# Optimization experiments

Hardware: AMD Instinct MI355X
Metric: run time of the kernel (lower is better)

## Reference

```python
import jax, jax.numpy as jnp
import numpy as np

N, D, V, T = 1024, 64, 32000, 2048
U_DECAY = 0.97
LN_EPS = 1e-6


def _layernorm_row(z):
    # matches torch: (z - mean) / (std_unbiased + eps), std uses ddof=1
    m = z.mean(axis=-1, keepdims=True)
    s = jnp.std(z, axis=-1, ddof=1, keepdims=True)
    return (z - m) / (s + LN_EPS)


def setup_inputs() -> dict:
    key = jax.random.key(0)
    k1, k2, k3, k4, k5 = jax.random.split(key, 5)
    E = jax.random.normal(k1, (D, N), dtype=jnp.float32) / np.float32(np.sqrt(N))
    Dx = jax.random.normal(k2, (N, D), dtype=jnp.float32) / np.float32(np.sqrt(D))
    Dy = jax.random.normal(k3, (N, D), dtype=jnp.float32) / np.float32(np.sqrt(D))
    token_emb = jax.random.normal(k4, (V, D), dtype=jnp.float32) / np.float32(np.sqrt(D))
    tokens = jax.random.randint(k5, (T,), 0, V, dtype=jnp.int32)
    x0 = jnp.zeros((N,), dtype=jnp.float32)
    rho0 = jnp.zeros((D, N), dtype=jnp.float32)
    return {"E": E, "Dx": Dx, "Dy": Dy, "token_emb": token_emb,
            "x0": x0, "rho0": rho0, "tokens": tokens}


def reference(E, Dx, Dy, token_emb, x0, rho0, tokens):
    def step(carry, tok):
        x, rho = carry                        # x: [N], rho: [D, N]
        v_prev = token_emb[tok]               # [D]
        x_t = x + jax.nn.relu(Dx @ v_prev)    # [N], use_relu_lowrank=True
        a_star = rho @ x_t                    # [D]
        y_core = Dy @ _layernorm_row(a_star)  # ln_before_Dy=True -> [N]
        y_t = jax.nn.relu(y_core) * jax.nn.relu(x_t)  # [N]
        v_star = _layernorm_row(E @ y_t)      # [D]
        rho_new = U_DECAY * (rho + jnp.outer(v_prev, x_t))  # [D, N]
        return (x_t, rho_new), (y_t, v_star)

    (_, _), (ys, vs) = jax.lax.scan(step, (x0, rho0), tokens)
    return ys, vs  # [T, N], [T, D]
```

## Files before the change

### kernel.cpp

```cpp
#include <hip/hip_runtime.h>
#include <math.h>

#define NN 1024
#define DD 64
#define TT 2048
#define UDEC 0.97f
#define EPS 1e-6f

#define CC 64
#define NCH 32
#define NSL 16
#define SLW 64
#define C2 8
#define NC2 256

#define NTHR 256

__device__ __forceinline__ int swz4(int r, int c4) { return r * 16 + (c4 ^ (r & 15)); }

#define DOT4(p, q2) ((p).x*(q2).x + (p).y*(q2).y + (p).z*(q2).z + (p).w*(q2).w)
#define F4ADD(a, b) make_float4((a).x+(b).x, (a).y+(b).y, (a).z+(b).z, (a).w+(b).w)

__global__ __launch_bounds__(NTHR) void k_prep(
    const float* __restrict__ E, float* __restrict__ Et4,
    const float* __restrict__ Dx, float* __restrict__ Dxq,
    const float* __restrict__ Dy, float* __restrict__ Dyq)
{
    const int b = blockIdx.x, tid = threadIdx.x;
    if (b < 64) {
        const int fi = b * NTHR + tid;
        const int n4 = fi >> 6, d = fi & 63;
        reinterpret_cast<float4*>(Et4)[fi] =
            reinterpret_cast<const float4*>(E)[d * (NN / 4) + n4];
    } else if (b < 128) {
        const int fi = (b - 64) * NTHR + tid;
        const int d4 = fi >> 10, n = fi & 1023;
        reinterpret_cast<float4*>(Dxq)[fi] =
            reinterpret_cast<const float4*>(Dx)[n * (DD / 4) + d4];
    } else {
        const int fi = (b - 128) * NTHR + tid;
        const int d4 = fi >> 10, n = fi & 1023;
        reinterpret_cast<float4*>(Dyq)[fi] =
            reinterpret_cast<const float4*>(Dy)[n * (DD / 4) + d4];
    }
}

__global__ __launch_bounds__(NTHR) void k_xscan(
    const float* __restrict__ Dxq, const float* __restrict__ temb,
    const int* __restrict__ toks, float* __restrict__ Xp, float* __restrict__ S)
{
    __shared__ float Vs[C2][DD];
    const int b = blockIdx.x, tid = threadIdx.x;
    const int cs = b >> 2, qx = b & 3;
    const int n = qx * 256 + tid;
    for (int i = tid; i < C2 * DD / 4; i += NTHR) {
        int s = i >> 4, d4 = i & 15;
        reinterpret_cast<float4*>(&Vs[s][0])[d4] =
            reinterpret_cast<const float4*>(temb + toks[cs * C2 + s] * DD)[d4];
    }
    __syncthreads();
    float dxr[DD];
    const float4* dxq4 = reinterpret_cast<const float4*>(Dxq);
#pragma unroll
    for (int j = 0; j < 16; ++j) {
        float4 v = dxq4[j * NN + n];
        dxr[4*j] = v.x; dxr[4*j+1] = v.y; dxr[4*j+2] = v.z; dxr[4*j+3] = v.w;
    }
    float run = 0.f;
    for (int s = 0; s < C2; ++s) {
        const float4* vr = reinterpret_cast<const float4*>(&Vs[s][0]);
        float a0 = 0.f, a1 = 0.f, a2 = 0.f, a3 = 0.f;
#pragma unroll
        for (int j = 0; j < 16; ++j) {
            float4 v = vr[j];
            a0 += v.x * dxr[4*j];     a1 += v.y * dxr[4*j+1];
            a2 += v.z * dxr[4*j+2];   a3 += v.w * dxr[4*j+3];
        }
        run += fmaxf((a0 + a1) + (a2 + a3), 0.f);
        Xp[(cs * C2 + s) * NN + n] = run;
    }
    S[cs * NN + n] = run;
}

__global__ __launch_bounds__(NTHR) void k_base(
    const float* __restrict__ S, const float* __restrict__ x0, float* __restrict__ Bb)
{
    __shared__ float ssl[8][33];
    const int b = blockIdx.x, tid = threadIdx.x;
    const int n_l = tid & 31, seg = tid >> 5;
    const int n = b * 32 + n_l;
    float m[32];
#pragma unroll
    for (int j = 0; j < 32; ++j) m[j] = S[(seg * 32 + j) * NN + n];
    float tot = 0.f;
#pragma unroll
    for (int j = 0; j < 32; ++j) tot += m[j];
    ssl[seg][n_l] = tot;
    __syncthreads();
    float acc = x0[n];
    for (int r = 0; r < seg; ++r) acc += ssl[r][n_l];
#pragma unroll
    for (int j = 0; j < 32; ++j) {
        Bb[(seg * 32 + j) * NN + n] = acc;
        acc += m[j];
    }
}

__global__ __launch_bounds__(NTHR) void k_mgram(
    const float* __restrict__ Xp, const float* __restrict__ Bb,
    const float* __restrict__ temb, const int* __restrict__ toks,
    float* __restrict__ M, float* __restrict__ Gp)
{
    __shared__ float Xs[CC * DD];
    __shared__ float Vw[CC * DD];
    __shared__ float pw[CC + 1];
    const int b = blockIdx.x, tid = threadIdx.x;
    const int c = b >> 5, q = (b >> 1) & 15, role = b & 1;
    if (role == 0 && tid <= CC) pw[tid] = powf(UDEC, (float)tid);
    for (int i = tid; i < CC * SLW / 4; i += NTHR) {
        int s = i >> 4, n4 = i & 15;
        int t = c * CC + s;
        float4 xv = *reinterpret_cast<const float4*>(&Xp[t * NN + q * SLW + n4 * 4]);
        float4 bv = *reinterpret_cast<const float4*>(&Bb[(t >> 3) * NN + q * SLW + n4 * 4]);
        reinterpret_cast<float4*>(Xs)[swz4(s, n4)] = F4ADD(xv, bv);
    }
    __syncthreads();
    if (role == 0) {
        for (int i = tid; i < CC * DD / 4; i += NTHR) {
            int s = i >> 4, d4 = i & 15;
            float4 v = reinterpret_cast<const float4*>(temb + toks[c * CC + s] * DD)[d4];
            float wv = pw[CC - s];
            reinterpret_cast<float4*>(Vw)[swz4(s, d4)] =
                make_float4(v.x * wv, v.y * wv, v.z * wv, v.w * wv);
        }
    }
    __syncthreads();
    const float4* Xs4 = reinterpret_cast<const float4*>(Xs);
    if (role == 0) {
        const int dg = tid >> 4, ng = tid & 15;
        float acc[16];
#pragma unroll
        for (int k = 0; k < 16; ++k) acc[k] = 0.f;
        const float4* Vw4 = reinterpret_cast<const float4*>(Vw);
        for (int s = 0; s < CC; ++s) {
            float4 vw = Vw4[swz4(s, dg)];
            float4 xs = Xs4[swz4(s, ng)];
            acc[0]  += vw.x*xs.x; acc[1]  += vw.x*xs.y; acc[2]  += vw.x*xs.z; acc[3]  += vw.x*xs.w;
            acc[4]  += vw.y*xs.x; acc[5]  += vw.y*xs.y; acc[6]  += vw.y*xs.z; acc[7]  += vw.y*xs.w;
            acc[8]  += vw.z*xs.x; acc[9]  += vw.z*xs.y; acc[10] += vw.z*xs.z; acc[11] += vw.z*xs.w;
            acc[12] += vw.w*xs.x; acc[13] += vw.w*xs.y; acc[14] += vw.w*xs.z; acc[15] += vw.w*xs.w;
        }
#pragma unroll
        for (int a = 0; a < 4; ++a)
            *reinterpret_cast<float4*>(&M[(c * DD + dg * 4 + a) * NN + q * SLW + ng * 4]) =
                make_float4(acc[a*4], acc[a*4+1], acc[a*4+2], acc[a*4+3]);
    } else {
        const int tg = tid >> 4, sg = tid & 15;
        float acc[16];
#pragma unroll
        for (int k = 0; k < 16; ++k) acc[k] = 0.f;
        for (int n4 = 0; n4 < 16; ++n4) {
            float4 xa[4], xb[4];
#pragma unroll
            for (int a = 0; a < 4; ++a) xa[a] = Xs4[swz4(tg * 4 + a, n4)];
#pragma unroll
            for (int e = 0; e < 4; ++e) xb[e] = Xs4[swz4(sg * 4 + e, n4)];
#pragma unroll
            for (int a = 0; a < 4; ++a)
#pragma unroll
                for (int e = 0; e < 4; ++e) acc[a*4+e] += DOT4(xa[a], xb[e]);
        }
        float* base = Gp + ((size_t)(c * NSL + q) * CC) * CC;
#pragma unroll
        for (int a = 0; a < 4; ++a)
            *reinterpret_cast<float4*>(base + (tg * 4 + a) * CC + sg * 4) =
                make_float4(acc[a*4], acc[a*4+1], acc[a*4+2], acc[a*4+3]);
    }
}

__global__ __launch_bounds__(NTHR) void k_rho(
    const float* __restrict__ M, const float* __restrict__ rho0, float* __restrict__ Rho)
{
    __shared__ float4 ssl[8][32];
    const int b = blockIdx.x, tid = threadIdx.x;
    const int l = tid & 31, seg = tid >> 5;
    const int f = b * 32 + l;
    const float uc  = powf(UDEC, (float)CC);
    const float uc4 = uc * uc * uc * uc;
    const float4* M4 = reinterpret_cast<const float4*>(M);
    float4 mreg[4];
#pragma unroll
    for (int j = 0; j < 4; ++j) mreg[j] = M4[(size_t)(seg * 4 + j) * (DD * NN / 4) + f];
    float4 ss = mreg[0];
#pragma unroll
    for (int j = 1; j < 4; ++j) {
        ss.x = fmaf(ss.x, uc, mreg[j].x); ss.y = fmaf(ss.y, uc, mreg[j].y);
        ss.z = fmaf(ss.z, uc, mreg[j].z); ss.w = fmaf(ss.w, uc, mreg[j].w);
    }
    ssl[seg][l] = ss;
    __syncthreads();
    float4 acc = reinterpret_cast<const float4*>(rho0)[f];
    for (int r = 0; r < seg; ++r) {
        float4 sv = ssl[r][l];
        acc.x = fmaf(acc.x, uc4, sv.x); acc.y = fmaf(acc.y, uc4, sv.y);
        acc.z = fmaf(acc.z, uc4, sv.z); acc.w = fmaf(acc.w, uc4, sv.w);
    }
    float4* R4 = reinterpret_cast<float4*>(Rho);
#pragma unroll
    for (int j = 0; j < 4; ++j) {
        R4[(size_t)(seg * 4 + j) * (DD * NN / 4) + f] = acc;
        acc.x = fmaf(acc.x, uc, mreg[j].x); acc.y = fmaf(acc.y, uc, mreg[j].y);
        acc.z = fmaf(acc.z, uc, mreg[j].z); acc.w = fmaf(acc.w, uc, mreg[j].w);
    }
}

__global__ __launch_bounds__(NTHR) void k_inter(
    const float* __restrict__ Xp, const float* __restrict__ Bb,
    const float* __restrict__ Rho, float* __restrict__ Pp)
{
    __shared__ float Xs[32 * DD];
    __shared__ float Rs[DD * DD];
    const int b = blockIdx.x, tid = threadIdx.x;
    const int c = b >> 5, q = (b >> 1) & 15, h = b & 1;
    for (int i = tid; i < 32 * SLW / 4; i += NTHR) {
        int s = i >> 4, n4 = i & 15;
        int t = c * CC + h * 32 + s;
        float4 xv = *reinterpret_cast<const float4*>(&Xp[t * NN + q * SLW + n4 * 4]);
        float4 bv = *reinterpret_cast<const float4*>(&Bb[(t >> 3) * NN + q * SLW + n4 * 4]);
        reinterpret_cast<float4*>(Xs)[swz4(s, n4)] = F4ADD(xv, bv);
    }
    for (int i = tid; i < DD * SLW / 4; i += NTHR) {
        int s = i >> 4, n4 = i & 15;
        reinterpret_cast<float4*>(Rs)[swz4(s, n4)] =
            *reinterpret_cast<const float4*>(&Rho[(size_t)(c * DD + s) * NN + q * SLW + n4 * 4]);
    }
    __syncthreads();
    const float4* Xs4 = reinterpret_cast<const float4*>(Xs);
    const float4* Rs4 = reinterpret_cast<const float4*>(Rs);
    const int ti = tid >> 4, dg = tid & 15;
    float acc[8];
#pragma unroll
    for (int k = 0; k < 8; ++k) acc[k] = 0.f;
    for (int n4 = 0; n4 < 16; ++n4) {
        float4 xa[2], rv[4];
#pragma unroll
        for (int a = 0; a < 2; ++a) xa[a] = Xs4[swz4(ti * 2 + a, n4)];
#pragma unroll
        for (int e = 0; e < 4; ++e) rv[e] = Rs4[swz4(dg * 4 + e, n4)];
#pragma unroll
        for (int a = 0; a < 2; ++a)
#pragma unroll
            for (int e = 0; e < 4; ++e) acc[a*4+e] += DOT4(xa[a], rv[e]);
    }
#pragma unroll
    for (int a = 0; a < 2; ++a) {
        int trow = h * 32 + ti * 2 + a;
        *reinterpret_cast<float4*>(
            Pp + (((size_t)(c * NSL + q) * CC) + trow) * DD + dg * 4) =
            make_float4(acc[a*4], acc[a*4+1], acc[a*4+2], acc[a*4+3]);
    }
}

__global__ __launch_bounds__(NTHR) void k_astar(
    const float* __restrict__ Gp, const float* __restrict__ Pp,
    const float* __restrict__ temb, const int* __restrict__ toks,
    float* __restrict__ LNA)
{
    __shared__ float Ve[CC * DD];
    __shared__ float Gt[4][CC];
    __shared__ float Pt[4][DD];
    __shared__ float pw[CC + 1];
    const int b = blockIdx.x, tid = threadIdx.x;
    const int c = b >> 4, sub = b & 15;
    if (tid <= CC) pw[tid] = powf(UDEC, (float)tid);
    for (int i = tid; i < CC * DD / 4; i += NTHR) {
        int s = i >> 4, d4 = i & 15;
        reinterpret_cast<float4*>(Ve)[s * 16 + d4] =
            reinterpret_cast<const float4*>(temb + toks[c * CC + s] * DD)[d4];
    }
    {
        int k = tid >> 6, s = tid & 63;
        int t = sub + 16 * k;
        float ag = 0.f, ap = 0.f;
#pragma unroll
        for (int q = 0; q < NSL; ++q) {
            ag += Gp[((size_t)(c * NSL + q) * CC + t) * CC + s];
            ap += Pp[((size_t)(c * NSL + q) * CC + t) * DD + s];
        }
        Gt[k][s] = ag; Pt[k][s] = ap;
    }
    __syncthreads();
    {
        const int tk = tid >> 6, d0 = tid & 63;
        const int t = sub + 16 * tk;
        float a = pw[t] * Pt[tk][d0];
        for (int s = 0; s < t; ++s)
            a = fmaf(pw[t - s] * Gt[tk][s], Ve[s * 64 + d0], a);
        float sum = a;
#pragma unroll
        for (int mm = 1; mm < 64; mm <<= 1) sum += __shfl_xor(sum, mm, 64);
        float mean = sum * (1.f / DD);
        float z = a - mean;
        float vv = z * z;
#pragma unroll
        for (int mm = 1; mm < 64; mm <<= 1) vv += __shfl_xor(vv, mm, 64);
        float inv = 1.f / (sqrtf(vv * (1.f / (DD - 1))) + EPS);
        LNA[(c * CC + t) * DD + d0] = z * inv;
    }
}

__global__ __launch_bounds__(NTHR) void k_y(
    const float* __restrict__ LNA, const float* __restrict__ Dyq,
    const float* __restrict__ Xp, const float* __restrict__ Bb,
    float* __restrict__ ys)
{
    __shared__ float L[8][DD];
    const int tt = blockIdx.y;
    const int n  = blockIdx.x * 256 + threadIdx.x;
    for (int i = threadIdx.x; i < 8 * DD / 4; i += NTHR)
        reinterpret_cast<float4*>(&L[0][0])[i] =
            reinterpret_cast<const float4*>(LNA + tt * 8 * DD)[i];
    __syncthreads();
    float dyr[DD];
    const float4* dyq4 = reinterpret_cast<const float4*>(Dyq);
#pragma unroll
    for (int j = 0; j < 16; ++j) {
        float4 v = dyq4[j * NN + n];
        dyr[4*j] = v.x; dyr[4*j+1] = v.y; dyr[4*j+2] = v.z; dyr[4*j+3] = v.w;
    }
#pragma unroll
    for (int t = 0; t < 8; ++t) {
        const float4* lr = reinterpret_cast<const float4*>(&L[t][0]);
        float a0 = 0.f, a1 = 0.f, a2 = 0.f, a3 = 0.f;
#pragma unroll
        for (int j = 0; j < 16; ++j) {
            float4 v = lr[j];
            a0 += v.x * dyr[4*j];   a1 += v.y * dyr[4*j+1];
            a2 += v.z * dyr[4*j+2]; a3 += v.w * dyr[4*j+3];
        }
        float yc = (a0 + a1) + (a2 + a3);
        int tg = tt * 8 + t;
        float xv = Xp[tg * NN + n] + Bb[(tg >> 3) * NN + n];
        ys[tg * NN + n] = fmaxf(yc, 0.f) * fmaxf(xv, 0.f);
    }
}

__global__ __launch_bounds__(NTHR) void k_v(
    const float* __restrict__ ys, const float* __restrict__ Et4, float* __restrict__ vs)
{
    __shared__ float Ys[4][NN];
    __shared__ float pre4[4][4][DD];
    __shared__ float pre[4][DD + 1];
    __shared__ float mrow[4], srow[4];
    const int tt = blockIdx.x, tid = threadIdx.x;
    for (int i = tid; i < NN; i += NTHR)
        reinterpret_cast<float4*>(&Ys[0][0])[i] =
            reinterpret_cast<const float4*>(ys + (size_t)tt * 4 * NN)[i];
    __syncthreads();
    const int w = tid >> 6, d = tid & 63;
    float a0 = 0.f, a1 = 0.f, a2 = 0.f, a3 = 0.f;
    const float4* et = reinterpret_cast<const float4*>(Et4) + (size_t)w * 64 * DD + d;
#pragma unroll 4
    for (int i = 0; i < 64; ++i) {
        float4 ev = et[(size_t)i * DD];
        const int n4g = (w * 64 + i) * 4;
        float4 y0 = *reinterpret_cast<const float4*>(&Ys[0][n4g]);
        float4 y1 = *reinterpret_cast<const float4*>(&Ys[1][n4g]);
        float4 y2 = *reinterpret_cast<const float4*>(&Ys[2][n4g]);
        float4 y3 = *reinterpret_cast<const float4*>(&Ys[3][n4g]);
        a0 += DOT4(ev, y0); a1 += DOT4(ev, y1);
        a2 += DOT4(ev, y2); a3 += DOT4(ev, y3);
    }
    pre4[w][0][d] = a0; pre4[w][1][d] = a1;
    pre4[w][2][d] = a2; pre4[w][3][d] = a3;
    __syncthreads();
    {
        const int k = tid >> 6, dd = tid & 63;
        pre[k][dd] = pre4[0][k][dd] + pre4[1][k][dd] + pre4[2][k][dd] + pre4[3][k][dd];
    }
    __syncthreads();
    if (tid < 4) {
        float m = 0.f;
#pragma unroll
        for (int dd2 = 0; dd2 < DD; ++dd2) m += pre[tid][dd2];
        m *= (1.f / DD);
        float v = 0.f;
#pragma unroll
        for (int dd2 = 0; dd2 < DD; ++dd2) { float z = pre[tid][dd2] - m; v += z * z; }
        mrow[tid] = m;
        srow[tid] = 1.f / (sqrtf(v * (1.f / (DD - 1))) + EPS);
    }
    __syncthreads();
    {
        int k = tid >> 6, dd = tid & 63;
        vs[(tt * 4 + k) * DD + dd] = (pre[k][dd] - mrow[k]) * srow[k];
    }
}

extern "C" void kernel_launch(void* const* d_in, const int* in_sizes, int n_in,
                              void* d_out, int out_size, void* d_ws, size_t ws_size,
                              hipStream_t stream) {
    (void)in_sizes; (void)n_in; (void)out_size; (void)ws_size;
    const float* E    = (const float*)d_in[0];
    const float* Dx   = (const float*)d_in[1];
    const float* Dy   = (const float*)d_in[2];
    const float* temb = (const float*)d_in[3];
    const float* x0   = (const float*)d_in[4];
    const float* rho0 = (const float*)d_in[5];
    const int*   toks = (const int*)d_in[6];

    float* ys = (float*)d_out;
    float* vs = ys + (size_t)TT * NN;

    float* w   = (float*)d_ws;
    float* Xp  = w;
    float* S   = Xp  + (size_t)TT * NN;
    float* Bb  = S   + (size_t)NC2 * NN;
    float* M   = Bb  + (size_t)NC2 * NN;
    float* Rho = M   + (size_t)NCH * DD * NN;
    float* Gp  = Rho + (size_t)NCH * DD * NN;
    float* LNA = Gp  + (size_t)NCH * NSL * CC * CC;
    float* Et4 = LNA + (size_t)TT * DD;
    float* Dxq = Et4 + (size_t)NN * DD;
    float* Dyq = Dxq + (size_t)NN * DD;
    float* Pp  = M;

    k_prep <<<dim3(192),       NTHR, 0, stream>>>(E, Et4, Dx, Dxq, Dy, Dyq);
    k_xscan<<<dim3(4 * NC2),   NTHR, 0, stream>>>(Dxq, temb, toks, Xp, S);
    k_base <<<dim3(32),        NTHR, 0, stream>>>(S, x0, Bb);
    k_mgram<<<dim3(NCH*NSL*2), NTHR, 0, stream>>>(Xp, Bb, temb, toks, M, Gp);
    k_rho  <<<dim3(512),       NTHR, 0, stream>>>(M, rho0, Rho);
    k_inter<<<dim3(NCH*NSL*2), NTHR, 0, stream>>>(Xp, Bb, Rho, Pp);
    k_astar<<<dim3(NCH*16),    NTHR, 0, stream>>>(Gp, Pp, temb, toks, LNA);
    k_y    <<<dim3(4, TT/8),   NTHR, 0, stream>>>(LNA, Dyq, Xp, Bb, ys);
    k_v    <<<dim3(TT/4),      NTHR, 0, stream>>>(ys, Et4, vs);
}
```

Before: 157.4 us.

## Split mgram and prep kernels and overlap independent work on a second stream

The combined M/Gram kernel is split into separate k_m and k_gram kernels. The Gram kernel and the E/Dy transposes now run on a second non-blocking stream, joined through events. The aim is to overlap independent work with the main dependency chain (xscan, M, rho, inter) and to avoid role-divergent blocks that allocate unused shared memory. The cost is extra launches and event synchronisation overhead. k_y also now depends on k_prep_rest through Dyq, but the second stream is not explicitly joined before k_y; it is only ordered indirectly via eGram, which is recorded after k_prep_rest on s2.

```diff
diff --git a/kernel.cpp b/kernel.cpp
--- a/kernel.cpp
+++ b/kernel.cpp
@@ -21,9 +21,17 @@
 #define DOT4(p, q2) ((p).x*(q2).x + (p).y*(q2).y + (p).z*(q2).z + (p).w*(q2).w)
 #define F4ADD(a, b) make_float4((a).x+(b).x, (a).y+(b).y, (a).z+(b).z, (a).w+(b).w)
 
-__global__ __launch_bounds__(NTHR) void k_prep(
+__global__ __launch_bounds__(NTHR) void k_prep_dx(
+    const float* __restrict__ Dx, float* __restrict__ Dxq)
+{
+    const int fi = blockIdx.x * NTHR + threadIdx.x;
+    const int d4 = fi >> 10, n = fi & 1023;
+    reinterpret_cast<float4*>(Dxq)[fi] =
+        reinterpret_cast<const float4*>(Dx)[n * (DD / 4) + d4];
+}
+
+__global__ __launch_bounds__(NTHR) void k_prep_rest(
     const float* __restrict__ E, float* __restrict__ Et4,
-    const float* __restrict__ Dx, float* __restrict__ Dxq,
     const float* __restrict__ Dy, float* __restrict__ Dyq)
 {
     const int b = blockIdx.x, tid = threadIdx.x;
@@ -32,13 +40,8 @@
         const int n4 = fi >> 6, d = fi & 63;
         reinterpret_cast<float4*>(Et4)[fi] =
             reinterpret_cast<const float4*>(E)[d * (NN / 4) + n4];
-    } else if (b < 128) {
+    } else {
         const int fi = (b - 64) * NTHR + tid;
-        const int d4 = fi >> 10, n = fi & 1023;
-        reinterpret_cast<float4*>(Dxq)[fi] =
-            reinterpret_cast<const float4*>(Dx)[n * (DD / 4) + d4];
-    } else {
-        const int fi = (b - 128) * NTHR + tid;
         const int d4 = fi >> 10, n = fi & 1023;
         reinterpret_cast<float4*>(Dyq)[fi] =
             reinterpret_cast<const float4*>(Dy)[n * (DD / 4) + d4];
@@ -106,17 +109,17 @@
     }
 }
 
-__global__ __launch_bounds__(NTHR) void k_mgram(
+__global__ __launch_bounds__(NTHR) void k_m(
     const float* __restrict__ Xp, const float* __restrict__ Bb,
     const float* __restrict__ temb, const int* __restrict__ toks,
-    float* __restrict__ M, float* __restrict__ Gp)
+    float* __restrict__ M)
 {
     __shared__ float Xs[CC * DD];
     __shared__ float Vw[CC * DD];
     __shared__ float pw[CC + 1];
     const int b = blockIdx.x, tid = threadIdx.x;
-    const int c = b >> 5, q = (b >> 1) & 15, role = b & 1;
-    if (role == 0 && tid <= CC) pw[tid] = powf(UDEC, (float)tid);
+    const int c = b >> 4, q = b & 15;
+    if (tid <= CC) pw[tid] = powf(UDEC, (float)tid);
     for (int i = tid; i < CC * SLW / 4; i += NTHR) {
         int s = i >> 4, n4 = i & 15;
         int t = c * CC + s;
@@ -125,57 +128,70 @@
         reinterpret_cast<float4*>(Xs)[swz4(s, n4)] = F4ADD(xv, bv);
     }
     __syncthreads();
-    if (role == 0) {
-        for (int i = tid; i < CC * DD / 4; i += NTHR) {
-            int s = i >> 4, d4 = i & 15;
-            float4 v = reinterpret_cast<const float4*>(temb + toks[c * CC + s] * DD)[d4];
-            float wv = pw[CC - s];
-            reinterpret_cast<float4*>(Vw)[swz4(s, d4)] =
-                make_float4(v.x * wv, v.y * wv, v.z * wv, v.w * wv);
-        }
+    for (int i = tid; i < CC * DD / 4; i += NTHR) {
+        int s = i >> 4, d4 = i & 15;
+        float4 v = reinterpret_cast<const float4*>(temb + toks[c * CC + s] * DD)[d4];
+        float wv = pw[CC - s];
+        reinterpret_cast<float4*>(Vw)[swz4(s, d4)] =
+            make_float4(v.x * wv, v.y * wv, v.z * wv, v.w * wv);
     }
     __syncthreads();
     const float4* Xs4 = reinterpret_cast<const float4*>(Xs);
-    if (role == 0) {
-        const int dg = tid >> 4, ng = tid & 15;
-        float acc[16];
-#pragma unroll
-        for (int k = 0; k < 16; ++k) acc[k] = 0.f;
-        const float4* Vw4 = reinterpret_cast<const float4*>(Vw);
-        for (int s = 0; s < CC; ++s) {
-            float4 vw = Vw4[swz4(s, dg)];
-            float4 xs = Xs4[swz4(s, ng)];
-            acc[0]  += vw.x*xs.x; acc[1]  += vw.x*xs.y; acc[2]  += vw.x*xs.z; acc[3]  += vw.x*xs.w;
-            acc[4]  += vw.y*xs.x; acc[5]  += vw.y*xs.y; acc[6]  += vw.y*xs.z; acc[7]  += vw.y*xs.w;
-            acc[8]  += vw.z*xs.x; acc[9]  += vw.z*xs.y; acc[10] += vw.z*xs.z; acc[11] += vw.z*xs.w;
-            acc[12] += vw.w*xs.x; acc[13] += vw.w*xs.y; acc[14] += vw.w*xs.z; acc[15] += vw.w*xs.w;
-        }
+    const float4* Vw4 = reinterpret_cast<const float4*>(Vw);
+    const int dg = tid >> 4, ng = tid & 15;
+    float acc[16];
+#pragma unroll
+    for (int k = 0; k < 16; ++k) acc[k] = 0.f;
+    for (int s = 0; s < CC; ++s) {
+        float4 vw = Vw4[swz4(s, dg)];
+        float4 xs = Xs4[swz4(s, ng)];
+        acc[0]  += vw.x*xs.x; acc[1]  += vw.x*xs.y; acc[2]  += vw.x*xs.z; acc[3]  += vw.x*xs.w;
+        acc[4]  += vw.y*xs.x; acc[5]  += vw.y*xs.y; acc[6]  += vw.y*xs.z; acc[7]  += vw.y*xs.w;
+        acc[8]  += vw.z*xs.x; acc[9]  += vw.z*xs.y; acc[10] += vw.z*xs.z; acc[11] += vw.z*xs.w;
+        acc[12] += vw.w*xs.x; acc[13] += vw.w*xs.y; acc[14] += vw.w*xs.z; acc[15] += vw.w*xs.w;
+    }
+#pragma unroll
+    for (int a = 0; a < 4; ++a)
+        *reinterpret_cast<float4*>(&M[(c * DD + dg * 4 + a) * NN + q * SLW + ng * 4]) =
+            make_float4(acc[a*4], acc[a*4+1], acc[a*4+2], acc[a*4+3]);
+}
+
+__global__ __launch_bounds__(NTHR) void k_gram(
+    const float* __restrict__ Xp, const float* __restrict__ Bb,
+    float* __restrict__ Gp)
+{
+    __shared__ float Xs[CC * DD];
+    const int b = blockIdx.x, tid = threadIdx.x;
+    const int c = b >> 4, q = b & 15;
+    for (int i = tid; i < CC * SLW / 4; i += NTHR) {
+        int s = i >> 4, n4 = i & 15;
+        int t = c * CC + s;
+        float4 xv = *reinterpret_cast<const float4*>(&Xp[t * NN + q * SLW + n4 * 4]);
+        float4 bv = *reinterpret_cast<const float4*>(&Bb[(t >> 3) * NN + q * SLW + n4 * 4]);
+        reinterpret_cast<float4*>(Xs)[swz4(s, n4)] = F4ADD(xv, bv);
+    }
+    __syncthreads();
+    const float4* Xs4 = reinterpret_cast<const float4*>(Xs);
+    const int tg = tid >> 4, sg = tid & 15;
+    float acc[16];
+#pragma unroll
+    for (int k = 0; k < 16; ++k) acc[k] = 0.f;
+    for (int n4 = 0; n4 < 16; ++n4) {
+        float4 xa[4], xb[4];
+#pragma unroll
+        for (int a = 0; a < 4; ++a) xa[a] = Xs4[swz4(tg * 4 + a, n4)];
+#pragma unroll
+        for (int e = 0; e < 4; ++e) xb[e] = Xs4[swz4(sg * 4 + e, n4)];
 #pragma unroll
         for (int a = 0; a < 4; ++a)
-            *reinterpret_cast<float4*>(&M[(c * DD + dg * 4 + a) * NN + q * SLW + ng * 4]) =
-                make_float4(acc[a*4], acc[a*4+1], acc[a*4+2], acc[a*4+3]);
-    } else {
-        const int tg = tid >> 4, sg = tid & 15;
-        float acc[16];
-#pragma unroll
-        for (int k = 0; k < 16; ++k) acc[k] = 0.f;
-        for (int n4 = 0; n4 < 16; ++n4) {
-            float4 xa[4], xb[4];
-#pragma unroll
-            for (int a = 0; a < 4; ++a) xa[a] = Xs4[swz4(tg * 4 + a, n4)];
-#pragma unroll
-            for (int e = 0; e < 4; ++e) xb[e] = Xs4[swz4(sg * 4 + e, n4)];
-#pragma unroll
-            for (int a = 0; a < 4; ++a)
-#pragma unroll
-                for (int e = 0; e < 4; ++e) acc[a*4+e] += DOT4(xa[a], xb[e]);
-        }
-        float* base = Gp + ((size_t)(c * NSL + q) * CC) * CC;
-#pragma unroll
-        for (int a = 0; a < 4; ++a)
-            *reinterpret_cast<float4*>(base + (tg * 4 + a) * CC + sg * 4) =
-                make_float4(acc[a*4], acc[a*4+1], acc[a*4+2], acc[a*4+3]);
-    }
+#pragma unroll
+            for (int e = 0; e < 4; ++e) acc[a*4+e] += DOT4(xa[a], xb[e]);
+    }
+    float* base = Gp + ((size_t)(c * NSL + q) * CC) * CC;
+#pragma unroll
+    for (int a = 0; a < 4; ++a)
+        *reinterpret_cast<float4*>(base + (tg * 4 + a) * CC + sg * 4) =
+            make_float4(acc[a*4], acc[a*4+1], acc[a*4+2], acc[a*4+3]);
 }
 
 __global__ __launch_bounds__(NTHR) void k_rho(
@@ -425,13 +441,33 @@
     float* Dyq = Dxq + (size_t)NN * DD;
     float* Pp  = M;
 
-    k_prep <<<dim3(192),       NTHR, 0, stream>>>(E, Et4, Dx, Dxq, Dy, Dyq);
-    k_xscan<<<dim3(4 * NC2),   NTHR, 0, stream>>>(Dxq, temb, toks, Xp, S);
-    k_base <<<dim3(32),        NTHR, 0, stream>>>(S, x0, Bb);
-    k_mgram<<<dim3(NCH*NSL*2), NTHR, 0, stream>>>(Xp, Bb, temb, toks, M, Gp);
-    k_rho  <<<dim3(512),       NTHR, 0, stream>>>(M, rho0, Rho);
-    k_inter<<<dim3(NCH*NSL*2), NTHR, 0, stream>>>(Xp, Bb, Rho, Pp);
-    k_astar<<<dim3(NCH*16),    NTHR, 0, stream>>>(Gp, Pp, temb, toks, LNA);
-    k_y    <<<dim3(4, TT/8),   NTHR, 0, stream>>>(LNA, Dyq, Xp, Bb, ys);
-    k_v    <<<dim3(TT/4),      NTHR, 0, stream>>>(ys, Et4, vs);
-}
+    static hipStream_t s2 = nullptr;
+    static hipEvent_t eFork = nullptr, eBase = nullptr, eGram = nullptr;
+    if (s2 == nullptr) {
+        hipStreamCreateWithFlags(&s2, hipStreamNonBlocking);
+        hipEventCreateWithFlags(&eFork, hipEventDisableTiming);
+        hipEventCreateWithFlags(&eBase, hipEventDisableTiming);
+        hipEventCreateWithFlags(&eGram, hipEventDisableTiming);
+    }
+
+    k_prep_dx<<<dim3(64),       NTHR, 0, stream>>>(Dx, Dxq);
+    hipEventRecord(eFork, stream);
+    hipStreamWaitEvent(s2, eFork, 0);
+    k_prep_rest<<<dim3(128),    NTHR, 0, s2>>>(E, Et4, Dy, Dyq);
+
+    k_xscan<<<dim3(4 * NC2),    NTHR, 0, stream>>>(Dxq, temb, toks, Xp, S);
+    k_base <<<dim3(32),         NTHR, 0, stream>>>(S, x0, Bb);
+    hipEventRecord(eBase, stream);
+    hipStreamWaitEvent(s2, eBase, 0);
+    k_gram <<<dim3(NCH * NSL),  NTHR, 0, s2>>>(Xp, Bb, Gp);
+    hipEventRecord(eGram, s2);
+
+    k_m    <<<dim3(NCH * NSL),  NTHR, 0, stream>>>(Xp, Bb, temb, toks, M);
+    k_rho  <<<dim3(512),        NTHR, 0, stream>>>(M, rho0, Rho);
+    k_inter<<<dim3(NCH*NSL*2),  NTHR, 0, stream>>>(Xp, Bb, Rho, Pp);
+
+    hipStreamWaitEvent(stream, eGram, 0);
+    k_astar<<<dim3(NCH * 16),   NTHR, 0, stream>>>(Gp, Pp, temb, toks, LNA);
+    k_y    <<<dim3(4, TT / 8),  NTHR, 0, stream>>>(LNA, Dyq, Xp, Bb, ys);
+    k_v    <<<dim3(TT / 4),     NTHR, 0, stream>>>(ys, Et4, vs);
+}
```

Result: slower. 205.6 us (+30.6%).
